# Kernel optimization log

Measured on AMD Instinct MI355X. Metric: run time of the kernel, lower is better.

The kernel has to match this reference:

```python
import jax, jax.numpy as jnp
import numpy as np

NUM_THRESH = 0.2
TEMP = 0.1


def setup_inputs() -> dict:
    key = jax.random.key(0)
    k1, k2 = jax.random.split(key)
    b, L, c = 8, 4096, 128  # L = h*w, h = w = 64
    feature1 = jax.random.normal(k1, (b, L, c), dtype=jnp.float32)
    feature2 = jax.random.normal(k2, (b, L, c), dtype=jnp.float32)
    return {"feature1": feature1, "feature2": feature2, "h": 64, "w": 64}


def reference(feature1, feature2, h, w):
    # similarity matrix [b, L, S]
    matrix = jnp.einsum('nlc,nsc->nls', feature1, feature2) / TEMP
    # dual softmax
    m = jax.nn.softmax(matrix, axis=1) * jax.nn.softmax(matrix, axis=2)
    # mutual-argmax mask with score threshold
    mask = (m > NUM_THRESH) \
        & (m == jnp.max(m, axis=2, keepdims=True)) \
        & (m == jnp.max(m, axis=1, keepdims=True))
    # torch mask.max(dim=2): values = any match in row, indices = first True (argmax of bool)
    mask_v = jnp.any(mask, axis=2)            # [b, L]
    j_ids = jnp.argmax(mask, axis=2)          # [b, L]
    # vectorized scatter-subtract: matched rows get f1[i] - f2[j]
    sub = jnp.take_along_axis(feature2, j_ids[..., None], axis=1)  # [b, L, c]
    featureout = jnp.where(mask_v[..., None], feature1 - sub, feature1)
    # rearrange 'n (h w) c -> n c h w'
    b, L, c = featureout.shape
    out = featureout.reshape(b, h, w, c).transpose(0, 3, 1, 2)
    return out
```

## Files before the change

kernel.cpp:

```cpp
#include <hip/hip_runtime.h>
#include <stdint.h>

typedef unsigned int uint32;
typedef unsigned long long u64;

#define BATCH 8
#define LDIM 4096
#define CDIM 128

typedef __attribute__((ext_vector_type(4))) int i32x4;
typedef __attribute__((ext_vector_type(16))) int i32x16;

#define DIG1_OFF  0ull
#define DIG2_OFF  16777216ull
#define RPF_OFF   33554432ull
#define CPF_OFF   37748736ull
#define LSER_OFF  41943040ull
#define LSEC_OFF  42205184ull
#define RPACK_OFF 42467328ull
#define CPACK_OFF 42729472ull
#define CCNT_OFF  42991616ull
#define CIDX_OFF  42995712ull
#define CT_OFF    45755712ull
#define WS_NEEDED 51380224ull

#define CAND_CAP 690000u
#define CMARGIN 2.40f

#define C1L (3.0517578125e-04 * 1.4426950408889634)
#define C2L (1.862645149230957e-08 * 1.4426950408889634)
#define LOG2_02 (-2.3219280948873623)

#define CROW(r, kgv) (((r)&3) + 8*((r)>>2) + 4*(kgv))

__device__ __forceinline__ uint32 fkey(float f) {
    uint32 u = __float_as_uint(f);
    return (u & 0x80000000u) ? ~u : (u | 0x80000000u);
}
__device__ __forceinline__ float keyf(uint32 k) {
    uint32 u = (k & 0x80000000u) ? (k ^ 0x80000000u) : ~k;
    return __uint_as_float(u);
}
__device__ __forceinline__ i32x16 mfma_i8(i32x4 a, i32x4 b, i32x16 c) {
    return __builtin_amdgcn_mfma_i32_32x32x32_i8(a, b, c, 0, 0, 0);
}
__device__ __forceinline__ void load_lds16(const char* g, char* l) {
    __builtin_amdgcn_global_load_lds((__attribute__((address_space(1))) void*)(g),
                                     (__attribute__((address_space(3))) void*)(l), 16, 0, 0);
}
__device__ __forceinline__ u64 umax64(u64 a, u64 b) { return a > b ? a : b; }

__global__ void fill_sentinel(float* out, int nelem) {
    int i = blockIdx.x * 256 + threadIdx.x;
    if (i < nelem) out[i] = 12345.0f;
}

__global__ void init_packs(u64* __restrict__ rowpack, u64* __restrict__ colpack,
                           uint32* __restrict__ ccount) {
    int idx = blockIdx.x * 256 + threadIdx.x;
    if (idx < BATCH * LDIM) { rowpack[idx] = 0ull; colpack[idx] = 0ull; }
    if (idx == 0) ccount[0] = 0u;
}

__global__ __launch_bounds__(256) void quant_kernel(const float* __restrict__ f1,
                                                    const float* __restrict__ f2,
                                                    char* __restrict__ dig)
{
    int tid = blockIdx.x * 256 + threadIdx.x;
    int l31 = tid & 31;
    int kg  = (tid >> 5) & 1;
    int kc  = (tid >> 6) & 3;
    int rb  = (tid >> 8) & 1;
    int blk = (tid >> 9) & 63;
    int n   = (tid >> 15) & 7;
    int inp = tid >> 18;
    int row = blk * 64 + rb * 32 + l31;

    const float* src = (inp ? f2 : f1) + ((size_t)(n * LDIM + row)) * CDIM + kc * 32 + kg * 16;
    char* dstc = dig + (inp ? DIG2_OFF : DIG1_OFF)
               + (((size_t)n * 64 + blk) * 4 + kc) * 8192;
    int gpos = rb * 64 + kg * 32 + l31;

    float4 v0 = ((const float4*)src)[0];
    float4 v1 = ((const float4*)src)[1];
    float4 v2 = ((const float4*)src)[2];
    float4 v3 = ((const float4*)src)[3];
    float xs[16] = {v0.x,v0.y,v0.z,v0.w, v1.x,v1.y,v1.z,v1.w,
                    v2.x,v2.y,v2.z,v2.w, v3.x,v3.y,v3.z,v3.w};
    uint32 wds[4][4] = {{0,0,0,0},{0,0,0,0},{0,0,0,0},{0,0,0,0}};
#pragma unroll
    for (int e = 0; e < 16; e++) {
        int q = __float2int_rn(xs[e] * 33554432.0f);
        int d0 = (q + (1 << 20)) >> 21; q -= d0 << 21;
        int d1 = (q + (1 << 13)) >> 14; q -= d1 << 14;
        int d2 = (q + (1 << 6)) >> 7;   q -= d2 << 7;
        int sh = (e & 3) * 8;
        wds[0][e >> 2] |= (uint32)(d0 & 255) << sh;
        wds[1][e >> 2] |= (uint32)(d1 & 255) << sh;
        wds[2][e >> 2] |= (uint32)(d2 & 255) << sh;
        wds[3][e >> 2] |= (uint32)(q  & 255) << sh;
    }
#pragma unroll
    for (int p = 0; p < 4; p++) {
        *(int4*)(dstc + (size_t)(p * 128 + gpos) * 16) =
            make_int4(wds[p][0], wds[p][1], wds[p][2], wds[p][3]);
    }
}

__global__ __launch_bounds__(512, 2) void gemm_fused(
    const char* __restrict__ dig,
    float* __restrict__ rpf, float* __restrict__ cpf,
    uint32* __restrict__ ccount, uint32* __restrict__ cidx, u64* __restrict__ ct)
{
    __shared__ __align__(16) char smp[75840];

    int wg = blockIdx.x;
    int swz = (wg & 7) * 1024 + (wg >> 3);
    int n  = swz >> 10;
    int tM = (swz >> 5) & 31;
    int tN = swz & 31;

    const int t = threadIdx.x;
    const int lane = t & 63, w = t >> 6;
    const int wr = w >> 2, wc = w & 3;
    const int l31 = lane & 31, kg = lane >> 5;

    const i32x16 zero16 = {0,0,0,0,0,0,0,0,0,0,0,0,0,0,0,0};
    i32x16 acc[2][4];
#pragma unroll
    for (int sm = 0; sm < 2; sm++)
#pragma unroll
        for (int k = 0; k < 4; k++) acc[sm][k] = zero16;

    auto stage_step = [&](int kc, int buf) {
#pragma unroll
        for (int i = 0; i < 4; i++) {
            int blk = (i < 2) ? (tM * 2 + i) : (tN * 2 + (i - 2));
            const char* src = dig + ((i < 2) ? DIG1_OFF : DIG2_OFF)
                            + (((size_t)n * 64 + blk) * 4 + kc) * 8192 + t * 16;
            load_lds16(src, smp + buf * 32768 + i * 8192 + t * 16);
        }
    };

    stage_step(0, 0);
    for (int kc = 0; kc < 4; kc++) {
        int buf = kc & 1;
        __syncthreads();
        if (kc < 3) stage_step(kc + 1, buf ^ 1);
        const char* Ab = smp + buf * 32768 + wr * 8192;
        const char* Bb = smp + buf * 32768 + 16384 + (wc >> 1) * 8192 + (wc & 1) * 1024;
        i32x4 aF[2][4], bF[4];
#pragma unroll
        for (int p = 0; p < 4; p++)
            bF[p] = *(const i32x4*)(Bb + p * 2048 + lane * 16);
#pragma unroll
        for (int sm = 0; sm < 2; sm++)
#pragma unroll
            for (int p = 0; p < 4; p++)
                aF[sm][p] = *(const i32x4*)(Ab + p * 2048 + sm * 1024 + lane * 16);
#pragma unroll
        for (int sm = 0; sm < 2; sm++) {
            acc[sm][0] = mfma_i8(aF[sm][0], bF[0], acc[sm][0]);
            acc[sm][1] = mfma_i8(aF[sm][0], bF[1], acc[sm][1]);
            acc[sm][1] = mfma_i8(aF[sm][1], bF[0], acc[sm][1]);
            acc[sm][2] = mfma_i8(aF[sm][0], bF[2], acc[sm][2]);
            acc[sm][2] = mfma_i8(aF[sm][1], bF[1], acc[sm][2]);
            acc[sm][2] = mfma_i8(aF[sm][2], bF[0], acc[sm][2]);
            acc[sm][3] = mfma_i8(aF[sm][0], bF[3], acc[sm][3]);
            acc[sm][3] = mfma_i8(aF[sm][1], bF[2], acc[sm][3]);
            acc[sm][3] = mfma_i8(aF[sm][2], bF[1], acc[sm][3]);
            acc[sm][3] = mfma_i8(aF[sm][3], bF[0], acc[sm][3]);
        }
    }

    const int col = wc * 32 + l31;

    int t01v[2][16], t23v[2][16];
    float lamf[2][16];
    const float c1f = (float)C1L, c2f = (float)C2L;
#pragma unroll
    for (int sm = 0; sm < 2; sm++)
#pragma unroll
        for (int r = 0; r < 16; r++) {
            t01v[sm][r] = acc[sm][0][r] * 128 + acc[sm][1][r];
            t23v[sm][r] = acc[sm][2][r] * 128 + acc[sm][3][r];
            lamf[sm][r] = fmaf((float)t23v[sm][r], c2f, (float)t01v[sm][r] * c1f);
        }

    float* trf = (float*)smp;
    float2* rstat = (float2*)(smp + 66560);
    float2* cpart = (float2*)(smp + 70656);
    float* rowMaxF = (float*)(smp + 74752);
    float* colMaxF = (float*)(smp + 75264);
    uint32* waveTot = (uint32*)(smp + 75776);

    __syncthreads();

#pragma unroll
    for (int sm = 0; sm < 2; sm++)
#pragma unroll
        for (int r = 0; r < 16; r++) {
            int row = wr * 64 + sm * 32 + CROW(r, kg);
            trf[row * 129 + col] = lamf[sm][r];
        }
    {
        float cm = lamf[0][0];
#pragma unroll
        for (int sm = 0; sm < 2; sm++)
#pragma unroll
            for (int r = 0; r < 16; r++) cm = fmaxf(cm, lamf[sm][r]);
        float cs = 0.f;
#pragma unroll
        for (int sm = 0; sm < 2; sm++)
#pragma unroll
            for (int r = 0; r < 16; r++) cs += exp2f(lamf[sm][r] - cm);
        cpart[(wr * 2 + kg) * 128 + col] = make_float2(cm, cs);
    }
    __syncthreads();

    {
        int row = t & 127, seg = t >> 7;
        const float* rp = trf + row * 129 + seg * 32;
        float v[32];
#pragma unroll
        for (int j = 0; j < 32; j++) v[j] = rp[j];
        float rm = v[0];
#pragma unroll
        for (int j = 1; j < 32; j++) rm = fmaxf(rm, v[j]);
        float rs = 0.f;
#pragma unroll
        for (int j = 0; j < 32; j++) rs += exp2f(v[j] - rm);
        rstat[seg * 128 + row] = make_float2(rm, rs);
    }
    __syncthreads();

    if (t < 128) {
        float2 a = rstat[t], b = rstat[128 + t], c = rstat[256 + t], d = rstat[384 + t];
        float M = fmaxf(fmaxf(a.x, b.x), fmaxf(c.x, d.x));
        float S = a.y * exp2f(a.x - M) + b.y * exp2f(b.x - M)
                + c.y * exp2f(c.x - M) + d.y * exp2f(d.x - M);
        rowMaxF[t] = M;
        rpf[((size_t)n * LDIM + tM * 128 + t) * 32 + tN] = M + log2f(S);
    } else if (t < 256) {
        int c0 = t - 128;
        float2 a = cpart[c0], b = cpart[128 + c0], c = cpart[256 + c0], d = cpart[384 + c0];
        float M = fmaxf(fmaxf(a.x, b.x), fmaxf(c.x, d.x));
        float S = a.y * exp2f(a.x - M) + b.y * exp2f(b.x - M)
                + c.y * exp2f(c.x - M) + d.y * exp2f(d.x - M);
        colMaxF[c0] = M;
        cpf[((size_t)n * LDIM + tN * 128 + c0) * 32 + tM] = M + log2f(S);
    }
    __syncthreads();

    uint32 mask = 0;
    {
        const float cthr = colMaxF[col] - CMARGIN;
#pragma unroll
        for (int sm = 0; sm < 2; sm++)
#pragma unroll
            for (int r = 0; r < 16; r++) {
                int row = wr * 64 + sm * 32 + CROW(r, kg);
                if (lamf[sm][r] >= rowMaxF[row] - CMARGIN && lamf[sm][r] >= cthr)
                    mask |= 1u << (sm * 16 + r);
            }
    }
    uint32 cnt = (uint32)__popc(mask);
    uint32 x = cnt;
#pragma unroll
    for (int d = 1; d < 64; d <<= 1) {
        uint32 y = __shfl_up(x, d);
        if (lane >= d) x += y;
    }
    if (lane == 63) waveTot[w] = x;
    __syncthreads();
    if (t == 0) {
        uint32 s = 0;
#pragma unroll
        for (int i = 0; i < 8; i++) { uint32 v = waveTot[i]; waveTot[i] = s; s += v; }
        waveTot[8] = s ? atomicAdd(ccount, s) : 0u;
    }
    __syncthreads();

    if (mask) {
        uint32 p = waveTot[8] + waveTot[w] + (x - cnt);
        const uint32 colG = (uint32)(tN * 128 + col);
#pragma unroll
        for (int sm = 0; sm < 2; sm++)
#pragma unroll
            for (int r = 0; r < 16; r++) {
                if (mask & (1u << (sm * 16 + r))) {
                    int row = wr * 64 + sm * 32 + CROW(r, kg);
                    if (p < CAND_CAP) {
                        cidx[p] = ((uint32)n << 24) | ((uint32)(tM * 128 + row) << 12) | colG;
                        ct[p] = ((u64)(uint32)t01v[sm][r] << 32) | (u64)(uint32)t23v[sm][r];
                    }
                    p++;
                }
            }
    }
}

__global__ __launch_bounds__(256) void merge_kernel(
    const float* __restrict__ rpf, const float* __restrict__ cpf,
    double* __restrict__ lse_row, double* __restrict__ lse_col)
{
    int idx = blockIdx.x * 256 + threadIdx.x;
    const float* src = (idx < BATCH * LDIM) ? rpf : cpf;
    double* dst = (idx < BATCH * LDIM) ? lse_row : lse_col;
    int i = idx & (BATCH * LDIM - 1);
    float M = -3.4e38f;
#pragma unroll
    for (int j = 0; j < 32; j++) M = fmaxf(M, src[(size_t)i * 32 + j]);
    double S = 0.0;
#pragma unroll
    for (int j = 0; j < 32; j++)
        S += exp2((double)src[(size_t)i * 32 + j] - (double)M);
    dst[i] = (double)M + log2(S);
}

__global__ __launch_bounds__(256) void finalize_kernel(
    const uint32* __restrict__ cidx, const u64* __restrict__ ct,
    const uint32* __restrict__ ccount,
    const double* __restrict__ lse_row, const double* __restrict__ lse_col,
    u64* __restrict__ rowpack, u64* __restrict__ colpack)
{
    uint32 cnt = ccount[0];
    if (cnt > CAND_CAP) cnt = CAND_CAP;
    uint32 i = blockIdx.x * 256 + threadIdx.x;
    if (i >= cnt) return;
    uint32 id = cidx[i];
    int n = id >> 24, rowG = (id >> 12) & 4095, colG = id & 4095;
    u64 tt = ct[i];
    int t01 = (int)(uint32)(tt >> 32), t23 = (int)(uint32)tt;
    double l2 = (double)t01 * C1L + (double)t23 * C2L;
    float gf = (float)(2.0 * l2 - lse_row[(size_t)n * LDIM + rowG]
                                - lse_col[(size_t)n * LDIM + colG]);
    u64 key = ((u64)fkey(gf)) << 32;
    atomicMax(&rowpack[(size_t)n * LDIM + rowG], key | (uint32)(~(uint32)colG));
    atomicMax(&colpack[(size_t)n * LDIM + colG], key | (uint32)(~(uint32)rowG));
}

__global__ __launch_bounds__(512, 2) void gemm_fallback(
    const char* __restrict__ dig, const uint32* __restrict__ ccount,
    const double* __restrict__ lse_row, const double* __restrict__ lse_col,
    u64* __restrict__ rowpack, u64* __restrict__ colpack)
{
    if (ccount[0] <= CAND_CAP) return;

    __shared__ __align__(16) char smp[68608];
    int wg = blockIdx.x;
    int swz = (wg & 7) * 1024 + (wg >> 3);
    int n  = swz >> 10;
    int tM = (swz >> 5) & 31;
    int tN = swz & 31;

    const int t = threadIdx.x;
    const int lane = t & 63, w = t >> 6;
    const int wr = w >> 2, wc = w & 3;
    const int l31 = lane & 31, kg = lane >> 5;

    double* lserd = (double*)(smp + 65536);
    double* lsecd = (double*)(smp + 66560);
    float*  lserf = (float*)(smp + 67584);
    float*  lsecf = (float*)(smp + 68096);
    if (t < 128) {
        double d = lse_row[(size_t)n * LDIM + tM * 128 + t];
        lserd[t] = d; lserf[t] = (float)d;
    } else if (t < 256) {
        int c = t - 128;
        double d = lse_col[(size_t)n * LDIM + tN * 128 + c];
        lsecd[c] = d; lsecf[c] = (float)d;
    }

    const i32x16 zero16 = {0,0,0,0,0,0,0,0,0,0,0,0,0,0,0,0};
    i32x16 acc[2][4];
#pragma unroll
    for (int sm = 0; sm < 2; sm++)
#pragma unroll
        for (int k = 0; k < 4; k++) acc[sm][k] = zero16;

    auto stage_step = [&](int kc, int buf) {
#pragma unroll
        for (int i = 0; i < 4; i++) {
            int blk = (i < 2) ? (tM * 2 + i) : (tN * 2 + (i - 2));
            const char* src = dig + ((i < 2) ? DIG1_OFF : DIG2_OFF)
                            + (((size_t)n * 64 + blk) * 4 + kc) * 8192 + t * 16;
            load_lds16(src, smp + buf * 32768 + i * 8192 + t * 16);
        }
    };

    stage_step(0, 0);
    for (int kc = 0; kc < 4; kc++) {
        int buf = kc & 1;
        __syncthreads();
        if (kc < 3) stage_step(kc + 1, buf ^ 1);
        const char* Ab = smp + buf * 32768 + wr * 8192;
        const char* Bb = smp + buf * 32768 + 16384 + (wc >> 1) * 8192 + (wc & 1) * 1024;
        i32x4 aF[2][4], bF[4];
#pragma unroll
        for (int p = 0; p < 4; p++)
            bF[p] = *(const i32x4*)(Bb + p * 2048 + lane * 16);
#pragma unroll
        for (int sm = 0; sm < 2; sm++)
#pragma unroll
            for (int p = 0; p < 4; p++)
                aF[sm][p] = *(const i32x4*)(Ab + p * 2048 + sm * 1024 + lane * 16);
#pragma unroll
        for (int sm = 0; sm < 2; sm++) {
            acc[sm][0] = mfma_i8(aF[sm][0], bF[0], acc[sm][0]);
            acc[sm][1] = mfma_i8(aF[sm][0], bF[1], acc[sm][1]);
            acc[sm][1] = mfma_i8(aF[sm][1], bF[0], acc[sm][1]);
            acc[sm][2] = mfma_i8(aF[sm][0], bF[2], acc[sm][2]);
            acc[sm][2] = mfma_i8(aF[sm][1], bF[1], acc[sm][2]);
            acc[sm][2] = mfma_i8(aF[sm][2], bF[0], acc[sm][2]);
            acc[sm][3] = mfma_i8(aF[sm][0], bF[3], acc[sm][3]);
            acc[sm][3] = mfma_i8(aF[sm][1], bF[2], acc[sm][3]);
            acc[sm][3] = mfma_i8(aF[sm][2], bF[1], acc[sm][3]);
            acc[sm][3] = mfma_i8(aF[sm][3], bF[0], acc[sm][3]);
        }
    }
    __syncthreads();

    const int col = wc * 32 + l31;
    const float two_c1f = (float)(2.0 * C1L);
    const float scol = lsecf[col] + (float)LOG2_02 - 17.0f;
    const double lcd = lsecd[col];
#pragma unroll
    for (int sm = 0; sm < 2; sm++)
#pragma unroll
        for (int r = 0; r < 16; r++) {
            int row = wr * 64 + sm * 32 + CROW(r, kg);
            int t01 = acc[sm][0][r] * 128 + acc[sm][1][r];
            float lv = (float)t01 * two_c1f;
            if (lv > lserf[row] + scol) {
                int t23 = acc[sm][2][r] * 128 + acc[sm][3][r];
                double l2 = (double)t01 * C1L + (double)t23 * C2L;
                float gf = (float)(2.0 * l2 - lserd[row] - lcd);
                u64 key = ((u64)fkey(gf)) << 32;
                atomicMax(&rowpack[(size_t)n * LDIM + tM * 128 + row],
                          key | (uint32)(~(uint32)(tN * 128 + col)));
                atomicMax(&colpack[(size_t)n * LDIM + tN * 128 + col],
                          key | (uint32)(~(uint32)(tM * 128 + row)));
            }
        }
}

__global__ __launch_bounds__(256) void out_kernel(
    const float* __restrict__ f1, const float* __restrict__ f2,
    const u64* __restrict__ rowpack, const u64* __restrict__ colpack,
    float* __restrict__ out)
{
    int n = blockIdx.y;
    int l0 = blockIdx.x * 64;
    int t = threadIdx.x;
    __shared__ int s_sh[64];
    __shared__ int m_sh[64];
    __shared__ float tile[64][129];
    if (t < 64) {
        u64 rp = rowpack[(size_t)n * LDIM + l0 + t];
        uint32 skey = (uint32)(rp >> 32);
        uint32 s = (~(uint32)rp) & 4095u;
        u64 cp = colpack[(size_t)n * LDIM + s];
        double g2 = (double)keyf(skey);
        int match = (((uint32)(cp >> 32)) == skey) && (g2 > LOG2_02);
        s_sh[t] = (int)s;
        m_sh[t] = match;
    }
    __syncthreads();
#pragma unroll
    for (int i = 0; i < 32; i++) {
        int idx = i * 256 + t;
        int lloc = idx >> 7, ch = idx & 127;
        float v = f1[((size_t)n * LDIM + l0 + lloc) * CDIM + ch];
        if (m_sh[lloc]) v -= f2[((size_t)n * LDIM + s_sh[lloc]) * CDIM + ch];
        tile[lloc][ch] = v;
    }
    __syncthreads();
#pragma unroll
    for (int i = 0; i < 32; i++) {
        int ch = i * 4 + (t >> 6), lw = t & 63;
        out[((size_t)n * CDIM + ch) * LDIM + l0 + lw] = tile[lw][ch];
    }
}

extern "C" void kernel_launch(void* const* d_in, const int* in_sizes, int n_in,
                              void* d_out, int out_size, void* d_ws, size_t ws_size,
                              hipStream_t stream)
{
    const float* f1 = (const float*)d_in[0];
    const float* f2 = (const float*)d_in[1];
    float* out = (float*)d_out;
    char* ws = (char*)d_ws;
    char* dig = ws;

    if (ws_size < WS_NEEDED) {
        fill_sentinel<<<(out_size + 255) / 256, 256, 0, stream>>>(out, out_size);
        return;
    }

    float* rpf      = (float*)(ws + RPF_OFF);
    float* cpf      = (float*)(ws + CPF_OFF);
    double* lse_row = (double*)(ws + LSER_OFF);
    double* lse_col = (double*)(ws + LSEC_OFF);
    u64* rowpack    = (u64*)(ws + RPACK_OFF);
    u64* colpack    = (u64*)(ws + CPACK_OFF);
    uint32* ccount  = (uint32*)(ws + CCNT_OFF);
    uint32* cidx    = (uint32*)(ws + CIDX_OFF);
    u64* ct         = (u64*)(ws + CT_OFF);

    quant_kernel<<<dim3(2048), dim3(256), 0, stream>>>(f1, f2, dig);
    init_packs<<<dim3(128), dim3(256), 0, stream>>>(rowpack, colpack, ccount);
    gemm_fused<<<dim3(8192), dim3(512), 0, stream>>>(dig, rpf, cpf, ccount, cidx, ct);
    merge_kernel<<<dim3(256), dim3(256), 0, stream>>>(rpf, cpf, lse_row, lse_col);
    finalize_kernel<<<dim3((CAND_CAP + 255) / 256), dim3(256), 0, stream>>>(
        cidx, ct, ccount, lse_row, lse_col, rowpack, colpack);
    gemm_fallback<<<dim3(8192), dim3(512), 0, stream>>>(
        dig, ccount, lse_row, lse_col, rowpack, colpack);
    out_kernel<<<dim3(LDIM / 64, BATCH), dim3(256), 0, stream>>>(
        f1, f2, rowpack, colpack, out);
}
```

Measured before the change: 404.3 us.

## Split fused GEMM tile across 16 waves with 32x32 per-wave subtiles

Doubles the gemm_fused workgroup from 512 to 1024 threads, so each wave computes a 32x32 output subtile instead of 64x32. Staging loads, the row-stat reduction (8 segments of 16 columns) and the column partials (8 partials) are rescaled to the new wave layout, and LDS grows to hold the larger stat arrays. The goal is more parallelism in the epilogue and a lighter per-wave register load. In exchange, each wave reuses fewer A fragments per MFMA, so LDS traffic per MFMA rises. The larger LDS footprint may also cap residency at one workgroup per CU, which gives the same total wave count as before.

```diff
diff --git a/kernel.cpp b/kernel.cpp
--- a/kernel.cpp
+++ b/kernel.cpp
@@ -107,12 +107,12 @@
     }
 }
 
-__global__ __launch_bounds__(512, 2) void gemm_fused(
+__global__ __launch_bounds__(1024, 4) void gemm_fused(
     const char* __restrict__ dig,
     float* __restrict__ rpf, float* __restrict__ cpf,
     uint32* __restrict__ ccount, uint32* __restrict__ cidx, u64* __restrict__ ct)
 {
-    __shared__ __align__(16) char smp[75840];
+    __shared__ __align__(16) char smp[84096];
 
     int wg = blockIdx.x;
     int swz = (wg & 7) * 1024 + (wg >> 3);
@@ -126,19 +126,20 @@
     const int l31 = lane & 31, kg = lane >> 5;
 
     const i32x16 zero16 = {0,0,0,0,0,0,0,0,0,0,0,0,0,0,0,0};
-    i32x16 acc[2][4];
-#pragma unroll
-    for (int sm = 0; sm < 2; sm++)
-#pragma unroll
-        for (int k = 0; k < 4; k++) acc[sm][k] = zero16;
+    i32x16 acc[4];
+#pragma unroll
+    for (int k = 0; k < 4; k++) acc[k] = zero16;
 
     auto stage_step = [&](int kc, int buf) {
 #pragma unroll
-        for (int i = 0; i < 4; i++) {
+        for (int q = 0; q < 2; q++) {
+            int g = t + q * 1024;
+            int i = g >> 9;
+            int within = g & 511;
             int blk = (i < 2) ? (tM * 2 + i) : (tN * 2 + (i - 2));
             const char* src = dig + ((i < 2) ? DIG1_OFF : DIG2_OFF)
-                            + (((size_t)n * 64 + blk) * 4 + kc) * 8192 + t * 16;
-            load_lds16(src, smp + buf * 32768 + i * 8192 + t * 16);
+                            + (((size_t)n * 64 + blk) * 4 + kc) * 8192 + within * 16;
+            load_lds16(src, smp + buf * 32768 + i * 8192 + within * 16);
         }
     };
 
@@ -147,106 +148,104 @@
         int buf = kc & 1;
         __syncthreads();
         if (kc < 3) stage_step(kc + 1, buf ^ 1);
-        const char* Ab = smp + buf * 32768 + wr * 8192;
+        const char* Ab = smp + buf * 32768 + (wr >> 1) * 8192 + (wr & 1) * 1024;
         const char* Bb = smp + buf * 32768 + 16384 + (wc >> 1) * 8192 + (wc & 1) * 1024;
-        i32x4 aF[2][4], bF[4];
-#pragma unroll
-        for (int p = 0; p < 4; p++)
+        i32x4 aF[4], bF[4];
+#pragma unroll
+        for (int p = 0; p < 4; p++) {
+            aF[p] = *(const i32x4*)(Ab + p * 2048 + lane * 16);
             bF[p] = *(const i32x4*)(Bb + p * 2048 + lane * 16);
-#pragma unroll
-        for (int sm = 0; sm < 2; sm++)
-#pragma unroll
-            for (int p = 0; p < 4; p++)
-                aF[sm][p] = *(const i32x4*)(Ab + p * 2048 + sm * 1024 + lane * 16);
-#pragma unroll
-        for (int sm = 0; sm < 2; sm++) {
-            acc[sm][0] = mfma_i8(aF[sm][0], bF[0], acc[sm][0]);
-            acc[sm][1] = mfma_i8(aF[sm][0], bF[1], acc[sm][1]);
-            acc[sm][1] = mfma_i8(aF[sm][1], bF[0], acc[sm][1]);
-            acc[sm][2] = mfma_i8(aF[sm][0], bF[2], acc[sm][2]);
-            acc[sm][2] = mfma_i8(aF[sm][1], bF[1], acc[sm][2]);
-            acc[sm][2] = mfma_i8(aF[sm][2], bF[0], acc[sm][2]);
-            acc[sm][3] = mfma_i8(aF[sm][0], bF[3], acc[sm][3]);
-            acc[sm][3] = mfma_i8(aF[sm][1], bF[2], acc[sm][3]);
-            acc[sm][3] = mfma_i8(aF[sm][2], bF[1], acc[sm][3]);
-            acc[sm][3] = mfma_i8(aF[sm][3], bF[0], acc[sm][3]);
-        }
+        }
+        acc[0] = mfma_i8(aF[0], bF[0], acc[0]);
+        acc[1] = mfma_i8(aF[0], bF[1], acc[1]);
+        acc[1] = mfma_i8(aF[1], bF[0], acc[1]);
+        acc[2] = mfma_i8(aF[0], bF[2], acc[2]);
+        acc[2] = mfma_i8(aF[1], bF[1], acc[2]);
+        acc[2] = mfma_i8(aF[2], bF[0], acc[2]);
+        acc[3] = mfma_i8(aF[0], bF[3], acc[3]);
+        acc[3] = mfma_i8(aF[1], bF[2], acc[3]);
+        acc[3] = mfma_i8(aF[2], bF[1], acc[3]);
+        acc[3] = mfma_i8(aF[3], bF[0], acc[3]);
     }
 
     const int col = wc * 32 + l31;
 
-    int t01v[2][16], t23v[2][16];
-    float lamf[2][16];
+    int t01v[16], t23v[16];
+    float lamf[16];
     const float c1f = (float)C1L, c2f = (float)C2L;
 #pragma unroll
-    for (int sm = 0; sm < 2; sm++)
-#pragma unroll
-        for (int r = 0; r < 16; r++) {
-            t01v[sm][r] = acc[sm][0][r] * 128 + acc[sm][1][r];
-            t23v[sm][r] = acc[sm][2][r] * 128 + acc[sm][3][r];
-            lamf[sm][r] = fmaf((float)t23v[sm][r], c2f, (float)t01v[sm][r] * c1f);
-        }
+    for (int r = 0; r < 16; r++) {
+        t01v[r] = acc[0][r] * 128 + acc[1][r];
+        t23v[r] = acc[2][r] * 128 + acc[3][r];
+        lamf[r] = fmaf((float)t23v[r], c2f, (float)t01v[r] * c1f);
+    }
 
     float* trf = (float*)smp;
     float2* rstat = (float2*)(smp + 66560);
-    float2* cpart = (float2*)(smp + 70656);
-    float* rowMaxF = (float*)(smp + 74752);
-    float* colMaxF = (float*)(smp + 75264);
-    uint32* waveTot = (uint32*)(smp + 75776);
-
-    __syncthreads();
-
-#pragma unroll
-    for (int sm = 0; sm < 2; sm++)
-#pragma unroll
-        for (int r = 0; r < 16; r++) {
-            int row = wr * 64 + sm * 32 + CROW(r, kg);
-            trf[row * 129 + col] = lamf[sm][r];
-        }
+    float2* cpart = (float2*)(smp + 74752);
+    float* rowMaxF = (float*)(smp + 82944);
+    float* colMaxF = (float*)(smp + 83456);
+    uint32* waveTot = (uint32*)(smp + 83968);
+
+    __syncthreads();
+
+#pragma unroll
+    for (int r = 0; r < 16; r++) {
+        int row = wr * 32 + CROW(r, kg);
+        trf[row * 129 + col] = lamf[r];
+    }
     {
-        float cm = lamf[0][0];
-#pragma unroll
-        for (int sm = 0; sm < 2; sm++)
-#pragma unroll
-            for (int r = 0; r < 16; r++) cm = fmaxf(cm, lamf[sm][r]);
+        float cm = lamf[0];
+#pragma unroll
+        for (int r = 1; r < 16; r++) cm = fmaxf(cm, lamf[r]);
         float cs = 0.f;
 #pragma unroll
-        for (int sm = 0; sm < 2; sm++)
-#pragma unroll
-            for (int r = 0; r < 16; r++) cs += exp2f(lamf[sm][r] - cm);
+        for (int r = 0; r < 16; r++) cs += exp2f(lamf[r] - cm);
         cpart[(wr * 2 + kg) * 128 + col] = make_float2(cm, cs);
     }
     __syncthreads();
 
     {
         int row = t & 127, seg = t >> 7;
-        const float* rp = trf + row * 129 + seg * 32;
-        float v[32];
-#pragma unroll
-        for (int j = 0; j < 32; j++) v[j] = rp[j];
+        const float* rp = trf + row * 129 + seg * 16;
+        float v[16];
+#pragma unroll
+        for (int j = 0; j < 16; j++) v[j] = rp[j];
         float rm = v[0];
 #pragma unroll
-        for (int j = 1; j < 32; j++) rm = fmaxf(rm, v[j]);
+        for (int j = 1; j < 16; j++) rm = fmaxf(rm, v[j]);
         float rs = 0.f;
 #pragma unroll
-        for (int j = 0; j < 32; j++) rs += exp2f(v[j] - rm);
+        for (int j = 0; j < 16; j++) rs += exp2f(v[j] - rm);
         rstat[seg * 128 + row] = make_float2(rm, rs);
     }
     __syncthreads();
 
     if (t < 128) {
-        float2 a = rstat[t], b = rstat[128 + t], c = rstat[256 + t], d = rstat[384 + t];
-        float M = fmaxf(fmaxf(a.x, b.x), fmaxf(c.x, d.x));
-        float S = a.y * exp2f(a.x - M) + b.y * exp2f(b.x - M)
-                + c.y * exp2f(c.x - M) + d.y * exp2f(d.x - M);
+        float2 p0 = rstat[t];
+        float M = p0.x;
+#pragma unroll
+        for (int i = 1; i < 8; i++) M = fmaxf(M, rstat[i * 128 + t].x);
+        float S = 0.f;
+#pragma unroll
+        for (int i = 0; i < 8; i++) {
+            float2 p = rstat[i * 128 + t];
+            S += p.y * exp2f(p.x - M);
+        }
         rowMaxF[t] = M;
         rpf[((size_t)n * LDIM + tM * 128 + t) * 32 + tN] = M + log2f(S);
     } else if (t < 256) {
         int c0 = t - 128;
-        float2 a = cpart[c0], b = cpart[128 + c0], c = cpart[256 + c0], d = cpart[384 + c0];
-        float M = fmaxf(fmaxf(a.x, b.x), fmaxf(c.x, d.x));
-        float S = a.y * exp2f(a.x - M) + b.y * exp2f(b.x - M)
-                + c.y * exp2f(c.x - M) + d.y * exp2f(d.x - M);
+        float2 p0 = cpart[c0];
+        float M = p0.x;
+#pragma unroll
+        for (int i = 1; i < 8; i++) M = fmaxf(M, cpart[i * 128 + c0].x);
+        float S = 0.f;
+#pragma unroll
+        for (int i = 0; i < 8; i++) {
+            float2 p = cpart[i * 128 + c0];
+            S += p.y * exp2f(p.x - M);
+        }
         colMaxF[c0] = M;
         cpf[((size_t)n * LDIM + tN * 128 + c0) * 32 + tM] = M + log2f(S);
     }
@@ -256,13 +255,11 @@
     {
         const float cthr = colMaxF[col] - CMARGIN;
 #pragma unroll
-        for (int sm = 0; sm < 2; sm++)
-#pragma unroll
-            for (int r = 0; r < 16; r++) {
-                int row = wr * 64 + sm * 32 + CROW(r, kg);
-                if (lamf[sm][r] >= rowMaxF[row] - CMARGIN && lamf[sm][r] >= cthr)
-                    mask |= 1u << (sm * 16 + r);
-            }
+        for (int r = 0; r < 16; r++) {
+            int row = wr * 32 + CROW(r, kg);
+            if (lamf[r] >= rowMaxF[row] - CMARGIN && lamf[r] >= cthr)
+                mask |= 1u << r;
+        }
     }
     uint32 cnt = (uint32)__popc(mask);
     uint32 x = cnt;
@@ -276,27 +273,25 @@
     if (t == 0) {
         uint32 s = 0;
 #pragma unroll
-        for (int i = 0; i < 8; i++) { uint32 v = waveTot[i]; waveTot[i] = s; s += v; }
-        waveTot[8] = s ? atomicAdd(ccount, s) : 0u;
+        for (int i = 0; i < 16; i++) { uint32 v = waveTot[i]; waveTot[i] = s; s += v; }
+        waveTot[16] = s ? atomicAdd(ccount, s) : 0u;
     }
     __syncthreads();
 
     if (mask) {
-        uint32 p = waveTot[8] + waveTot[w] + (x - cnt);
+        uint32 p = waveTot[16] + waveTot[w] + (x - cnt);
         const uint32 colG = (uint32)(tN * 128 + col);
 #pragma unroll
-        for (int sm = 0; sm < 2; sm++)
-#pragma unroll
-            for (int r = 0; r < 16; r++) {
-                if (mask & (1u << (sm * 16 + r))) {
-                    int row = wr * 64 + sm * 32 + CROW(r, kg);
-                    if (p < CAND_CAP) {
-                        cidx[p] = ((uint32)n << 24) | ((uint32)(tM * 128 + row) << 12) | colG;
-                        ct[p] = ((u64)(uint32)t01v[sm][r] << 32) | (u64)(uint32)t23v[sm][r];
-                    }
-                    p++;
+        for (int r = 0; r < 16; r++) {
+            if (mask & (1u << r)) {
+                int row = wr * 32 + CROW(r, kg);
+                if (p < CAND_CAP) {
+                    cidx[p] = ((uint32)n << 24) | ((uint32)(tM * 128 + row) << 12) | colG;
+                    ct[p] = ((u64)(uint32)t01v[r] << 32) | (u64)(uint32)t23v[r];
                 }
+                p++;
             }
+        }
     }
 }
 
@@ -510,7 +505,7 @@
 
     quant_kernel<<<dim3(2048), dim3(256), 0, stream>>>(f1, f2, dig);
     init_packs<<<dim3(128), dim3(256), 0, stream>>>(rowpack, colpack, ccount);
-    gemm_fused<<<dim3(8192), dim3(512), 0, stream>>>(dig, rpf, cpf, ccount, cidx, ct);
+    gemm_fused<<<dim3(8192), dim3(1024), 0, stream>>>(dig, rpf, cpf, ccount, cidx, ct);
     merge_kernel<<<dim3(256), dim3(256), 0, stream>>>(rpf, cpf, lse_row, lse_col);
     finalize_kernel<<<dim3((CAND_CAP + 255) / 256), dim3(256), 0, stream>>>(
         cidx, ct, ccount, lse_row, lse_col, rowpack, colpack);
```

After: 371.3 us. 8.2% less time.
